# Performance work log

Hardware: AMD Instinct MI355X
Metric: run time of the kernel (lower is better)

Reference implementation:

```python
import jax, jax.numpy as jnp
import numpy as np

T, N, DEG = 8, 8192, 15
H = 4


def _gat(x, src, dst, wl, wr, a, b):
    """GATv2Conv with concat=False (heads averaged). x: [N, Cin] -> [N, Cout].
    e_ij = a_h . LeakyReLU(Wl x_j + Wr x_i); softmax over incoming edges of i;
    messages are Wl x_j (PyG GATv2 convention, self-loops already in edge list)."""
    n = x.shape[0]
    h, c = a.shape
    gl = (x @ wl).reshape(n, h, c)  # source-side transform
    gr = (x @ wr).reshape(n, h, c)  # target-side transform
    z = jax.nn.leaky_relu(gl[src] + gr[dst], 0.2)          # [E,H,C]
    e = jnp.einsum('ehc,hc->eh', z, a)                     # [E,H]
    m = jax.ops.segment_max(e, dst, num_segments=n)        # [N,H]
    ex = jnp.exp(e - m[dst])
    den = jax.ops.segment_sum(ex, dst, num_segments=n)     # [N,H]
    msg = jax.ops.segment_sum(ex[:, :, None] * gl[src], dst, num_segments=n)
    return (msg / den[:, :, None]).mean(axis=1) + b


def _d3(x, esrc, edst, wl, wr, a, b):
    # spatio-temporal graph conv: GATv2 applied independently per timestep
    return jax.lax.map(lambda args: _gat(args[0], args[1], args[2], wl, wr, a, b),
                       (x, esrc, edst))


def setup_inputs() -> dict:
    key = jax.random.key(0)
    ks = iter(jax.random.split(key, 32))
    x = jax.random.normal(next(ks), (T, N, 64), dtype=jnp.float32)
    # fixed-degree random graph per timestep + self loops (PyG add_self_loops=True)
    dst_base = jnp.repeat(jnp.arange(N, dtype=jnp.int32), DEG)
    src_r = jax.random.randint(next(ks), (T, N * DEG), 0, N, dtype=jnp.int32)
    loop = jnp.arange(N, dtype=jnp.int32)
    edge_src = jnp.concatenate([src_r, jnp.broadcast_to(loop, (T, N))], axis=1)
    edge_dst = jnp.concatenate([jnp.broadcast_to(dst_base, (T, N * DEG)),
                                jnp.broadcast_to(loop, (T, N))], axis=1)

    def gat_p(k, cin, cout):
        k1, k2, k3 = jax.random.split(k, 3)
        s = 1.0 / np.sqrt(cin)
        return ((jax.random.normal(k1, (cin, H * cout)) * s).astype(jnp.float32),
                (jax.random.normal(k2, (cin, H * cout)) * s).astype(jnp.float32),
                (jax.random.normal(k3, (H, cout)) * s).astype(jnp.float32),
                jnp.zeros((cout,), jnp.float32))

    inp = {"x": x, "edge_src": edge_src, "edge_dst": edge_dst}
    for name, cin, cout in [("c1", 64, 128), ("c2", 128, 64), ("c3", 64, 64), ("c4", 128, 64),
                            ("r11", 64, 64), ("r12", 64, 64), ("r2", 128, 128),
                            ("f11", 64, 64), ("f2", 128, 128)]:
        wl, wr, a, b = gat_p(next(ks), cin, cout)
        inp[name + "_wl"], inp[name + "_wr"], inp[name + "_a"], inp[name + "_b"] = wl, wr, a, b
    # ConvTranspose1d(k=1) == per-node linear conv_ch -> in_channels; then Linear in_channels -> original_dim
    for name, cin, cout in [("r3", 128, 64), ("f3", 128, 64), ("r4", 64, 64), ("f4", 64, 64)]:
        inp[name + "_w"] = (jax.random.normal(next(ks), (cin, cout)) * (1.0 / np.sqrt(cin))).astype(jnp.float32)
        inp[name + "_b"] = jnp.zeros((cout,), jnp.float32)
    return inp


def reference(x, edge_src, edge_dst,
              c1_wl, c1_wr, c1_a, c1_b, c2_wl, c2_wr, c2_a, c2_b,
              c3_wl, c3_wr, c3_a, c3_b, c4_wl, c4_wr, c4_a, c4_b,
              r11_wl, r11_wr, r11_a, r11_b, r12_wl, r12_wr, r12_a, r12_b,
              r2_wl, r2_wr, r2_a, r2_b, r3_w, r3_b, r4_w, r4_b,
              f11_wl, f11_wr, f11_a, f11_b, f2_wl, f2_wr, f2_a, f2_b,
              f3_w, f3_b, f4_w, f4_b):
    elu = jax.nn.elu
    out = elu(_d3(x, edge_src, edge_dst, c1_wl, c1_wr, c1_a, c1_b))           # [T,N,128]
    emb = elu(_d3(out, edge_src, edge_dst, c2_wl, c2_wr, c2_a, c2_b))         # [T,N,64]
    emb = elu(jnp.concatenate([_d3(emb, edge_src, edge_dst, c3_wl, c3_wr, c3_a, c3_b), emb], -1))  # [T,N,128]
    emb = elu(_d3(emb, edge_src, edge_dst, c4_wl, c4_wr, c4_a, c4_b))         # [T,N,64]

    # reconstruction branch on edges at t = -1
    s1, d1 = edge_src[-1], edge_dst[-1]
    r = elu(_gat(emb[-1], s1, d1, r11_wl, r11_wr, r11_a, r11_b))
    r = elu(jnp.concatenate([_gat(r, s1, d1, r12_wl, r12_wr, r12_a, r12_b), r], -1))  # [N,128]
    # F.dropout in eval mode -> identity
    r = elu(_gat(r, s1, d1, r2_wl, r2_wr, r2_a, r2_b))
    r = jnp.tanh(r @ r3_w + r3_b)
    recon = r @ r4_w + r4_b

    # forecasting branch on edges at t = -2 (original reuses reconstruct12 here)
    s2, d2 = edge_src[-2], edge_dst[-2]
    f = elu(_gat(emb[-2], s2, d2, f11_wl, f11_wr, f11_a, f11_b))
    f = elu(jnp.concatenate([_gat(f, s2, d2, r12_wl, r12_wr, r12_a, r12_b), f], -1))
    f = elu(_gat(f, s2, d2, f2_wl, f2_wr, f2_a, f2_b))
    f = jnp.tanh(f @ f3_w + f3_b)
    forecast = f @ f4_w + f4_b
    return (recon, forecast, emb)
```

## Files before the change

### kernel.cpp

```cpp
#include <hip/hip_runtime.h>
#include <cmath>

constexpr int T_   = 8;
constexpr int N_   = 8192;
constexpr int DEG_ = 15;
constexpr int E_   = N_ * (DEG_ + 1);
constexpr float L2E_ = 1.44269504f;

__device__ __forceinline__ float elu1(float v) {
  return v > 0.f ? v : exp2f(v * L2E_) - 1.f;
}

typedef __attribute__((ext_vector_type(8))) short bf16x8;
typedef __attribute__((ext_vector_type(4))) float f32x4;

__device__ __forceinline__ ushort f2bf(float x) {
  uint u = __float_as_uint(x);
  return (ushort)((u + 0x7FFFu + ((u >> 16) & 1u)) >> 16);
}
__device__ __forceinline__ float bf2f(ushort h) {
  return __uint_as_float(((uint)h) << 16);
}

template<int CTRL>
__device__ __forceinline__ float dpp_add(float x) {
  const int t = __builtin_amdgcn_mov_dpp(__float_as_int(x), CTRL, 0xf, 0xf, true);
  return x + __int_as_float(t);
}
__device__ __forceinline__ float row_reduce16(float x) {
  x = dpp_add<0x121>(x);
  x = dpp_add<0x122>(x);
  x = dpp_add<0x124>(x);
  x = dpp_add<0x128>(x);
  return x;
}

__global__ __launch_bounds__(256) void split_x(
    const float* __restrict__ X, ushort* __restrict__ XH, ushort* __restrict__ XL, int n4)
{
  const int i = blockIdx.x * 256 + threadIdx.x;
  if (i >= n4) return;
  const float4 v = ((const float4*)X)[i];
  const ushort h0 = f2bf(v.x), h1 = f2bf(v.y), h2 = f2bf(v.z), h3 = f2bf(v.w);
  ushort4 hh; hh.x = h0; hh.y = h1; hh.z = h2; hh.w = h3;
  ushort4 ll;
  ll.x = f2bf(v.x - bf2f(h0)); ll.y = f2bf(v.y - bf2f(h1));
  ll.z = f2bf(v.z - bf2f(h2)); ll.w = f2bf(v.w - bf2f(h3));
  ((ushort4*)XH)[i] = hh;
  ((ushort4*)XL)[i] = ll;
}

__global__ __launch_bounds__(256) void split_wt(
    const float* __restrict__ Wl, const float* __restrict__ Wr,
    ushort* __restrict__ WH, ushort* __restrict__ WL, int K, int HC)
{
  const int idx = blockIdx.x * 256 + threadIdx.x;
  if (idx >= 2 * HC * K) return;
  const int k = idx % K;
  const int n = (idx / K) % HC;
  const int s = idx / (K * HC);
  const float v = (s ? Wr : Wl)[k * HC + n];
  const ushort h = f2bf(v);
  WH[idx] = h;
  WL[idx] = f2bf(v - bf2f(h));
}

__global__ __launch_bounds__(256) void gemm_mfma(
    const ushort* __restrict__ Ah, const ushort* __restrict__ Al,
    const ushort* __restrict__ Wh, const ushort* __restrict__ Wl,
    float* __restrict__ Cl, float* __restrict__ Cr,
    int M, int Ncol, int K, int nt)
{
  __shared__ alignas(16) ushort lAh[4 * 1032];
  __shared__ alignas(16) ushort lAl[4 * 1032];
  __shared__ alignas(16) ushort lBh[4 * 520];
  __shared__ alignas(16) ushort lBl[4 * 520];

  const int z = blockIdx.z;
  const int t = (z < nt) ? z : z - nt;
  const int side = (z < nt) ? 0 : 1;
  const ushort* __restrict__ Bh = Wh + (size_t)side * Ncol * K;
  const ushort* __restrict__ Bl = Wl + (size_t)side * Ncol * K;
  float* __restrict__ C = (side ? Cr : Cl) + (size_t)t * M * Ncol;
  const size_t aoff = (size_t)t * M * K;

  const int bm = blockIdx.x * 128, bn = blockIdx.y * 64;
  const int tid = threadIdx.x;
  const int wid = tid >> 6, lane = tid & 63;
  const int l15 = lane & 15, lk = lane >> 4;

  f32x4 acc[2][4] = {};

  for (int k0 = 0; k0 < K; k0 += 32) {
    #pragma unroll
    for (int c = 0; c < 2; c++) {
      const int ch = tid + c * 256;
      const int row = ch >> 2, kc = ch & 3;
      const size_t ga = aoff + (size_t)(bm + row) * K + (k0 + kc * 8);
      *(uint4*)&lAh[kc * 1032 + row * 8] = *(const uint4*)(Ah + ga);
      *(uint4*)&lAl[kc * 1032 + row * 8] = *(const uint4*)(Al + ga);
    }
    {
      const int col = tid >> 2, kc = tid & 3;
      const size_t gb = (size_t)(bn + col) * K + (k0 + kc * 8);
      *(uint4*)&lBh[kc * 520 + col * 8] = *(const uint4*)(Bh + gb);
      *(uint4*)&lBl[kc * 520 + col * 8] = *(const uint4*)(Bl + gb);
    }
    __syncthreads();

    bf16x8 ah[2], al[2], bh4[4], bl4[4];
    const int r0 = wid * 32;
    #pragma unroll
    for (int rf = 0; rf < 2; rf++) {
      const int ro = (r0 + rf * 16 + l15) * 8;
      ah[rf] = *(const bf16x8*)&lAh[lk * 1032 + ro];
      al[rf] = *(const bf16x8*)&lAl[lk * 1032 + ro];
    }
    #pragma unroll
    for (int cf = 0; cf < 4; cf++) {
      const int co = (cf * 16 + l15) * 8;
      bh4[cf] = *(const bf16x8*)&lBh[lk * 520 + co];
      bl4[cf] = *(const bf16x8*)&lBl[lk * 520 + co];
    }
    #pragma unroll
    for (int rf = 0; rf < 2; rf++)
      #pragma unroll
      for (int cf = 0; cf < 4; cf++) {
        acc[rf][cf] = __builtin_amdgcn_mfma_f32_16x16x32_bf16(ah[rf], bh4[cf], acc[rf][cf], 0, 0, 0);
        acc[rf][cf] = __builtin_amdgcn_mfma_f32_16x16x32_bf16(ah[rf], bl4[cf], acc[rf][cf], 0, 0, 0);
        acc[rf][cf] = __builtin_amdgcn_mfma_f32_16x16x32_bf16(al[rf], bh4[cf], acc[rf][cf], 0, 0, 0);
      }
    __syncthreads();
  }

  #pragma unroll
  for (int rf = 0; rf < 2; rf++)
    #pragma unroll
    for (int cf = 0; cf < 4; cf++) {
      const int col = bn + cf * 16 + l15;
      #pragma unroll
      for (int reg = 0; reg < 4; reg++) {
        const int row = bm + wid * 32 + rf * 16 + lk * 4 + reg;
        C[(size_t)row * Ncol + col] = acc[rf][cf][reg];
      }
    }
}

template<int EPI>
__global__ __launch_bounds__(256) void gemm_k(
    const float* __restrict__ A, const float* __restrict__ B,
    float* __restrict__ C, const float* __restrict__ bias,
    int M, int Ncol, int K)
{
  __shared__ float As[16][68];
  __shared__ float Bs[16][64];

  const int tid = threadIdx.x;
  const int tx = tid & 15, ty = tid >> 4;
  const int bm = blockIdx.x * 64, bn = blockIdx.y * 64;

  const int arow = tid >> 2;
  const int akc  = (tid & 3) * 4;
  const int brow = tid >> 4;
  const int bc4  = (tid & 15) * 4;

  float acc[4][4];
  #pragma unroll
  for (int i = 0; i < 4; i++)
    #pragma unroll
    for (int j = 0; j < 4; j++) acc[i][j] = 0.f;

  for (int k0 = 0; k0 < K; k0 += 16) {
    const float4 va = *(const float4*)(A + (size_t)(bm + arow) * K + (k0 + akc));
    const float4 vb = *(const float4*)(B + (size_t)(k0 + brow) * Ncol + (bn + bc4));
    As[akc + 0][arow] = va.x; As[akc + 1][arow] = va.y;
    As[akc + 2][arow] = va.z; As[akc + 3][arow] = va.w;
    *(float4*)&Bs[brow][bc4] = vb;
    __syncthreads();
    #pragma unroll
    for (int kk = 0; kk < 16; kk++) {
      const float4 av = *(const float4*)&As[kk][ty * 4];
      const float4 bv = *(const float4*)&Bs[kk][tx * 4];
      const float a4[4] = {av.x, av.y, av.z, av.w};
      const float b4[4] = {bv.x, bv.y, bv.z, bv.w};
      #pragma unroll
      for (int i = 0; i < 4; i++)
        #pragma unroll
        for (int j = 0; j < 4; j++)
          acc[i][j] = fmaf(a4[i], b4[j], acc[i][j]);
    }
    __syncthreads();
  }

  #pragma unroll
  for (int i = 0; i < 4; i++) {
    const int row = bm + ty * 4 + i;
    const int col = bn + tx * 4;
    float v[4] = {acc[i][0], acc[i][1], acc[i][2], acc[i][3]};
    #pragma unroll
    for (int j = 0; j < 4; j++) v[j] += bias[col + j];
    if (EPI == 1) {
      #pragma unroll
      for (int j = 0; j < 4; j++) v[j] = tanhf(v[j]);
    }
    *(float4*)(C + (size_t)row * Ncol + col) = make_float4(v[0], v[1], v[2], v[3]);
  }
}

template<bool CONCAT, bool WF32>
__global__ __launch_bounds__(256) void gat_agg256(
    const float* __restrict__ GL, const float* __restrict__ GR,
    const float* __restrict__ aw_, const float* __restrict__ bias,
    const int* __restrict__ esrc, float* __restrict__ out,
    const float* __restrict__ csrc,
    ushort* __restrict__ SHo, ushort* __restrict__ SLo, int numNodes)
{
  constexpr int HC = 256, C = 64;
  constexpr int OSTR = CONCAT ? 128 : 64;

  const int lane = threadIdx.x & 63;
  const int wid  = threadIdx.x >> 6;
  const int t    = blockIdx.x >> 11;
  const int gid  = blockIdx.x * 4 + wid;
  if (gid >= numNodes) return;
  const int i = gid & (N_ - 1);

  const float* __restrict__ gl = GL + (size_t)t * N_ * HC;
  const int*   __restrict__ es = esrc + (size_t)t * E_ + (size_t)i * DEG_;
  const uint lo16 = (uint)lane << 4;

  float gr[4], a6[4], a4c[4];
  {
    const float4 gv = *(const float4*)(GR + (size_t)gid * HC + lane * 4);
    const float4 av = *(const float4*)(aw_ + lane * 4);
    gr[0] = gv.x; gr[1] = gv.y; gr[2] = gv.z; gr[3] = gv.w;
    a6[0] = 0.6f * L2E_ * av.x; a6[1] = 0.6f * L2E_ * av.y;
    a6[2] = 0.6f * L2E_ * av.z; a6[3] = 0.6f * L2E_ * av.w;
    a4c[0] = 0.4f * L2E_ * av.x; a4c[1] = 0.4f * L2E_ * av.y;
    a4c[2] = 0.4f * L2E_ * av.z; a4c[3] = 0.4f * L2E_ * av.w;
  }

  float acc[4] = {0.f, 0.f, 0.f, 0.f};
  float den = 0.f, m = -1e30f;

  #pragma unroll
  for (int b = 0; b < 4; b++) {
    uint off[4];
    #pragma unroll
    for (int q = 0; q < 4; q++) {
      const int ek = b * 4 + q;
      const uint j = (uint)((ek < DEG_) ? es[ek] : i);
      off[q] = (j << 10) + lo16;
    }
    float g[4][4];
    #pragma unroll
    for (int q = 0; q < 4; q++) {
      const float4 v = *(const float4*)((const char*)gl + off[q]);
      g[q][0] = v.x; g[q][1] = v.y; g[q][2] = v.z; g[q][3] = v.w;
    }
    float p[4];
    #pragma unroll
    for (int q = 0; q < 4; q++) {
      float s = 0.f;
      #pragma unroll
      for (int u = 0; u < 4; u++) {
        const float z = g[q][u] + gr[u];
        s = fmaf(z, a6[u], s);
        s = fmaf(fabsf(z), a4c[u], s);
      }
      p[q] = s;
    }
    #pragma unroll
    for (int q = 0; q < 4; q++) p[q] = row_reduce16(p[q]);

    const float bmax = fmaxf(fmaxf(p[0], p[1]), fmaxf(p[2], p[3]));
    const float nm   = fmaxf(m, bmax);
    const float sc   = exp2f(m - nm);
    den *= sc;
    #pragma unroll
    for (int u = 0; u < 4; u++) acc[u] *= sc;
    #pragma unroll
    for (int q = 0; q < 4; q++) {
      const float w = exp2f(p[q] - nm);
      den += w;
      #pragma unroll
      for (int u = 0; u < 4; u++) acc[u] = fmaf(w, g[q][u], acc[u]);
    }
    m = nm;
  }

  const float inv = 0.25f / den;
  #pragma unroll
  for (int u = 0; u < 4; u++) acc[u] *= inv;
  #pragma unroll
  for (int u = 0; u < 4; u++) {
    acc[u] += __shfl_xor(acc[u], 16);
    acc[u] += __shfl_xor(acc[u], 32);
  }

  if (lane < 16) {
    float o[4];
    #pragma unroll
    for (int u = 0; u < 4; u++)
      o[u] = elu1(acc[u] + bias[lane * 4 + u]);
    if (WF32)
      *(float4*)(out + (size_t)gid * OSTR + lane * 4) = make_float4(o[0], o[1], o[2], o[3]);
    ushort4 hh, ll;
    hh.x = f2bf(o[0]); hh.y = f2bf(o[1]); hh.z = f2bf(o[2]); hh.w = f2bf(o[3]);
    ll.x = f2bf(o[0] - bf2f(hh.x)); ll.y = f2bf(o[1] - bf2f(hh.y));
    ll.z = f2bf(o[2] - bf2f(hh.z)); ll.w = f2bf(o[3] - bf2f(hh.w));
    *(ushort4*)(SHo + (size_t)gid * OSTR + lane * 4) = hh;
    *(ushort4*)(SLo + (size_t)gid * OSTR + lane * 4) = ll;
  } else if (CONCAT && lane < 32) {
    const int q = lane - 16;
    const float4 v = *(const float4*)(csrc + (size_t)gid * C + q * 4);
    const float o0 = elu1(v.x), o1 = elu1(v.y), o2 = elu1(v.z), o3 = elu1(v.w);
    if (WF32)
      *(float4*)(out + (size_t)gid * OSTR + C + q * 4) = make_float4(o0, o1, o2, o3);
    ushort4 hh, ll;
    hh.x = f2bf(o0); hh.y = f2bf(o1); hh.z = f2bf(o2); hh.w = f2bf(o3);
    ll.x = f2bf(o0 - bf2f(hh.x)); ll.y = f2bf(o1 - bf2f(hh.y));
    ll.z = f2bf(o2 - bf2f(hh.z)); ll.w = f2bf(o3 - bf2f(hh.w));
    *(ushort4*)(SHo + (size_t)gid * OSTR + C + q * 4) = hh;
    *(ushort4*)(SLo + (size_t)gid * OSTR + C + q * 4) = ll;
  }
}

template<bool WF32, bool SPLIT>
__global__ __launch_bounds__(256) void gat_agg512(
    const float* __restrict__ GL, const float* __restrict__ GR,
    const float* __restrict__ aw_, const float* __restrict__ bias,
    const int* __restrict__ esrc, float* __restrict__ out,
    ushort* __restrict__ SHo, ushort* __restrict__ SLo)
{
  __shared__ float smem[4][128];

  const int lane = threadIdx.x & 63;
  const int h    = threadIdx.x >> 6;
  const int gid  = blockIdx.x;
  const int t = gid >> 13;
  const int i = gid & (N_ - 1);

  const float* __restrict__ gl = GL + (size_t)t * N_ * 512;
  const int*   __restrict__ es = esrc + (size_t)t * E_ + (size_t)i * DEG_;
  const int cb = h * 128 + lane * 2;
  const uint cbo = (uint)cb << 2;

  float gr0, gr1, a60, a61, a40, a41;
  {
    const float2 gv = *(const float2*)(GR + (size_t)gid * 512 + cb);
    const float2 av = *(const float2*)(aw_ + cb);
    gr0 = gv.x; gr1 = gv.y;
    a60 = 0.6f * L2E_ * av.x; a61 = 0.6f * L2E_ * av.y;
    a40 = 0.4f * L2E_ * av.x; a41 = 0.4f * L2E_ * av.y;
  }

  float acc0 = 0.f, acc1 = 0.f, den = 0.f, m = -1e30f;

  #pragma unroll
  for (int b = 0; b < 4; b++) {
    uint off[4];
    #pragma unroll
    for (int q = 0; q < 4; q++) {
      const int ek = b * 4 + q;
      const uint j = (uint)((ek < DEG_) ? es[ek] : i);
      off[q] = (j << 11) + cbo;
    }
    float g[4][2];
    #pragma unroll
    for (int q = 0; q < 4; q++) {
      const float2 v = *(const float2*)((const char*)gl + off[q]);
      g[q][0] = v.x; g[q][1] = v.y;
    }
    float p[4];
    #pragma unroll
    for (int q = 0; q < 4; q++) {
      const float z0 = g[q][0] + gr0;
      const float z1 = g[q][1] + gr1;
      float s = z0 * a60;
      s = fmaf(fabsf(z0), a40, s);
      s = fmaf(z1, a61, s);
      s = fmaf(fabsf(z1), a41, s);
      p[q] = s;
    }
    #pragma unroll
    for (int q = 0; q < 4; q++) {
      p[q] = row_reduce16(p[q]);
      p[q] += __shfl_xor(p[q], 16);
      p[q] += __shfl_xor(p[q], 32);
    }
    const float bmax = fmaxf(fmaxf(p[0], p[1]), fmaxf(p[2], p[3]));
    const float nm   = fmaxf(m, bmax);
    const float sc   = exp2f(m - nm);
    den *= sc; acc0 *= sc; acc1 *= sc;
    #pragma unroll
    for (int q = 0; q < 4; q++) {
      const float w = exp2f(p[q] - nm);
      den += w;
      acc0 = fmaf(w, g[q][0], acc0);
      acc1 = fmaf(w, g[q][1], acc1);
    }
    m = nm;
  }

  const float inv = 0.25f / den;
  smem[h][lane * 2]     = acc0 * inv;
  smem[h][lane * 2 + 1] = acc1 * inv;
  __syncthreads();

  if (h == 0) {
    const int c = lane * 2;
    float s0 = smem[0][c] + smem[1][c] + smem[2][c] + smem[3][c];
    float s1 = smem[0][c + 1] + smem[1][c + 1] + smem[2][c + 1] + smem[3][c + 1];
    s0 = elu1(s0 + bias[c]);
    s1 = elu1(s1 + bias[c + 1]);
    if (WF32)
      *(float2*)(out + (size_t)gid * 128 + c) = make_float2(s0, s1);
    if (SPLIT) {
      ushort2 hh, ll;
      hh.x = f2bf(s0); hh.y = f2bf(s1);
      ll.x = f2bf(s0 - bf2f(hh.x)); ll.y = f2bf(s1 - bf2f(hh.y));
      *(ushort2*)(SHo + (size_t)gid * 128 + c) = hh;
      *(ushort2*)(SLo + (size_t)gid * 128 + c) = ll;
    }
  }
}

extern "C" void kernel_launch(void* const* d_in, const int* in_sizes, int n_in,
                              void* d_out, int out_size, void* d_ws, size_t ws_size,
                              hipStream_t stream)
{
  (void)in_sizes; (void)n_in; (void)out_size; (void)ws_size;

  const float* x  = (const float*)d_in[0];
  const int*   es = (const int*)d_in[1];
  const float *c1_wl=(const float*)d_in[3], *c1_wr=(const float*)d_in[4], *c1_a=(const float*)d_in[5], *c1_b=(const float*)d_in[6];
  const float *c2_wl=(const float*)d_in[7], *c2_wr=(const float*)d_in[8], *c2_a=(const float*)d_in[9], *c2_b=(const float*)d_in[10];
  const float *c3_wl=(const float*)d_in[11],*c3_wr=(const float*)d_in[12],*c3_a=(const float*)d_in[13],*c3_b=(const float*)d_in[14];
  const float *c4_wl=(const float*)d_in[15],*c4_wr=(const float*)d_in[16],*c4_a=(const float*)d_in[17],*c4_b=(const float*)d_in[18];
  const float *r11_wl=(const float*)d_in[19],*r11_wr=(const float*)d_in[20],*r11_a=(const float*)d_in[21],*r11_b=(const float*)d_in[22];
  const float *r12_wl=(const float*)d_in[23],*r12_wr=(const float*)d_in[24],*r12_a=(const float*)d_in[25],*r12_b=(const float*)d_in[26];
  const float *r2_wl=(const float*)d_in[27],*r2_wr=(const float*)d_in[28],*r2_a=(const float*)d_in[29],*r2_b=(const float*)d_in[30];
  const float *f11_wl=(const float*)d_in[31],*f11_wr=(const float*)d_in[32],*f11_a=(const float*)d_in[33],*f11_b=(const float*)d_in[34];
  const float *f2_wl=(const float*)d_in[35],*f2_wr=(const float*)d_in[36],*f2_a=(const float*)d_in[37],*f2_b=(const float*)d_in[38];
  const float *r3_w=(const float*)d_in[39], *r3_b=(const float*)d_in[40];
  const float *f3_w=(const float*)d_in[41], *f3_b=(const float*)d_in[42];
  const float *r4_w=(const float*)d_in[43], *r4_b=(const float*)d_in[44];
  const float *f4_w=(const float*)d_in[45], *f4_b=(const float*)d_in[46];

  float* ws = (float*)d_ws;
  float* GL = ws;
  float* GR = GL + (size_t)16777216;
  float* A1 = GR + (size_t)16777216;
  float* B0 = A1 + (size_t)T_ * N_ * 64;
  float* B1 = B0 + (size_t)N_ * 128;
  ushort* SH  = (ushort*)(B1 + (size_t)N_ * 128);
  ushort* SL  = SH + (size_t)8388608;
  ushort* SH2 = SL + (size_t)8388608;
  ushort* SL2 = SH2 + (size_t)8388608;
  ushort* WH  = SL2 + (size_t)8388608;
  ushort* WL  = WH + (size_t)131072;

  float* recon = (float*)d_out;
  float* fcst  = recon + (size_t)N_ * 64;
  float* emb   = fcst + (size_t)N_ * 64;

  const dim3 blk(256);

  split_x<<<dim3(T_ * N_ * 64 / 4 / 256), blk, 0, stream>>>(x, SH, SL, T_ * N_ * 64 / 4);
  split_wt<<<dim3((2 * 512 * 64 + 255) / 256), blk, 0, stream>>>(c1_wl, c1_wr, WH, WL, 64, 512);
  for (int ch = 0; ch < 2; ch++) {
    const int t0 = ch * 4, nt = 4;
    gemm_mfma<<<dim3(N_ / 128, 8, 2 * nt), blk, 0, stream>>>(
        SH + (size_t)t0 * N_ * 64, SL + (size_t)t0 * N_ * 64, WH, WL, GL, GR, N_, 512, 64, nt);
    gat_agg512<false, true><<<dim3(nt * N_), blk, 0, stream>>>(
        GL, GR, c1_a, c1_b, es + (size_t)t0 * E_, nullptr,
        SH2 + (size_t)t0 * N_ * 128, SL2 + (size_t)t0 * N_ * 128);
  }
  split_wt<<<dim3((2 * 256 * 128 + 255) / 256), blk, 0, stream>>>(c2_wl, c2_wr, WH, WL, 128, 256);
  gemm_mfma<<<dim3(N_ / 128, 4, 2 * T_), blk, 0, stream>>>(SH2, SL2, WH, WL, GL, GR, N_, 256, 128, T_);
  gat_agg256<false, true><<<dim3(T_ * N_ / 4), blk, 0, stream>>>(
      GL, GR, c2_a, c2_b, es, A1, nullptr, SH, SL, T_ * N_);
  split_wt<<<dim3((2 * 256 * 64 + 255) / 256), blk, 0, stream>>>(c3_wl, c3_wr, WH, WL, 64, 256);
  gemm_mfma<<<dim3(N_ / 128, 4, 2 * T_), blk, 0, stream>>>(SH, SL, WH, WL, GL, GR, N_, 256, 64, T_);
  gat_agg256<true, false><<<dim3(T_ * N_ / 4), blk, 0, stream>>>(
      GL, GR, c3_a, c3_b, es, nullptr, A1, SH, SL, T_ * N_);
  split_wt<<<dim3((2 * 256 * 128 + 255) / 256), blk, 0, stream>>>(c4_wl, c4_wr, WH, WL, 128, 256);
  gemm_mfma<<<dim3(N_ / 128, 4, 2 * T_), blk, 0, stream>>>(SH, SL, WH, WL, GL, GR, N_, 256, 128, T_);
  gat_agg256<false, true><<<dim3(T_ * N_ / 4), blk, 0, stream>>>(
      GL, GR, c4_a, c4_b, es, emb, nullptr, SH2, SL2, T_ * N_);

  const int* esR = es + (size_t)7 * E_;
  split_wt<<<dim3((2 * 256 * 64 + 255) / 256), blk, 0, stream>>>(r11_wl, r11_wr, WH, WL, 64, 256);
  gemm_mfma<<<dim3(N_ / 128, 4, 2), blk, 0, stream>>>(
      SH2 + (size_t)7 * N_ * 64, SL2 + (size_t)7 * N_ * 64, WH, WL, GL, GR, N_, 256, 64, 1);
  gat_agg256<false, true><<<dim3(N_ / 4), blk, 0, stream>>>(
      GL, GR, r11_a, r11_b, esR, B0, nullptr, SH, SL, N_);
  split_wt<<<dim3((2 * 256 * 64 + 255) / 256), blk, 0, stream>>>(r12_wl, r12_wr, WH, WL, 64, 256);
  gemm_mfma<<<dim3(N_ / 128, 4, 2), blk, 0, stream>>>(SH, SL, WH, WL, GL, GR, N_, 256, 64, 1);
  gat_agg256<true, false><<<dim3(N_ / 4), blk, 0, stream>>>(
      GL, GR, r12_a, r12_b, esR, nullptr, B0, SH, SL, N_);
  split_wt<<<dim3((2 * 512 * 128 + 255) / 256), blk, 0, stream>>>(r2_wl, r2_wr, WH, WL, 128, 512);
  gemm_mfma<<<dim3(N_ / 128, 8, 2), blk, 0, stream>>>(SH, SL, WH, WL, GL, GR, N_, 512, 128, 1);
  gat_agg512<true, false><<<dim3(N_), blk, 0, stream>>>(GL, GR, r2_a, r2_b, esR, B0, nullptr, nullptr);
  gemm_k<1><<<dim3(N_ / 64, 1, 1), blk, 0, stream>>>(B0, r3_w, B1, r3_b, N_, 64, 128);
  gemm_k<2><<<dim3(N_ / 64, 1, 1), blk, 0, stream>>>(B1, r4_w, recon, r4_b, N_, 64, 64);

  const int* esF = es + (size_t)6 * E_;
  split_wt<<<dim3((2 * 256 * 64 + 255) / 256), blk, 0, stream>>>(f11_wl, f11_wr, WH, WL, 64, 256);
  gemm_mfma<<<dim3(N_ / 128, 4, 2), blk, 0, stream>>>(
      SH2 + (size_t)6 * N_ * 64, SL2 + (size_t)6 * N_ * 64, WH, WL, GL, GR, N_, 256, 64, 1);
  gat_agg256<false, true><<<dim3(N_ / 4), blk, 0, stream>>>(
      GL, GR, f11_a, f11_b, esF, B0, nullptr, SH, SL, N_);
  split_wt<<<dim3((2 * 256 * 64 + 255) / 256), blk, 0, stream>>>(r12_wl, r12_wr, WH, WL, 64, 256);
  gemm_mfma<<<dim3(N_ / 128, 4, 2), blk, 0, stream>>>(SH, SL, WH, WL, GL, GR, N_, 256, 64, 1);
  gat_agg256<true, false><<<dim3(N_ / 4), blk, 0, stream>>>(
      GL, GR, r12_a, r12_b, esF, nullptr, B0, SH, SL, N_);
  split_wt<<<dim3((2 * 512 * 128 + 255) / 256), blk, 0, stream>>>(f2_wl, f2_wr, WH, WL, 128, 512);
  gemm_mfma<<<dim3(N_ / 128, 8, 2), blk, 0, stream>>>(SH, SL, WH, WL, GL, GR, N_, 512, 128, 1);
  gat_agg512<true, false><<<dim3(N_), blk, 0, stream>>>(GL, GR, f2_a, f2_b, esF, B0, nullptr, nullptr);
  gemm_k<1><<<dim3(N_ / 64, 1, 1), blk, 0, stream>>>(B0, f3_w, B1, f3_b, N_, 64, 128);
  gemm_k<2><<<dim3(N_ / 64, 1, 1), blk, 0, stream>>>(B1, f4_w, fcst, f4_b, N_, 64, 64);
}
```

Baseline: 1.011 ms.

## Pad edge lists, batch weight splits, and remap 512-wide GAT aggregation to one wave per node

Adds a pre-pass that packs each node's 15 neighbours plus its self-loop into a 16-entry aligned array, so aggregation kernels load indices with uint4 reads instead of scalar loads and a branch. All nine weight bf16 hi/lo splits are merged into one launch with a table of offsets, which cuts many small kernel launches. gat_agg512 changes from a 4-wave block per node with a shared-memory head reduction to one wave per node, each lane covering 8 channels, which removes __syncthreads and LDS traffic. The online softmax skips the rescale on the first block. The cost is extra edge-index memory plus one more kernel, and higher register use in the 512 kernel.

```diff
diff --git a/kernel.cpp b/kernel.cpp
--- a/kernel.cpp
+++ b/kernel.cpp
@@ -33,6 +33,24 @@
   x = dpp_add<0x124>(x);
   x = dpp_add<0x128>(x);
   return x;
+}
+
+__global__ __launch_bounds__(256) void pad_edges(
+    const int* __restrict__ es, uint* __restrict__ es16, int total)
+{
+  const int idx = blockIdx.x * 256 + threadIdx.x;
+  if (idx >= total) return;
+  const int t = idx >> 13, i = idx & (N_ - 1);
+  const int* e = es + (size_t)t * E_ + (size_t)i * DEG_;
+  uint o[16];
+  #pragma unroll
+  for (int k = 0; k < DEG_; k++) o[k] = (uint)e[k];
+  o[15] = (uint)i;
+  uint4* dst = (uint4*)(es16 + (size_t)idx * 16);
+  dst[0] = make_uint4(o[0], o[1], o[2], o[3]);
+  dst[1] = make_uint4(o[4], o[5], o[6], o[7]);
+  dst[2] = make_uint4(o[8], o[9], o[10], o[11]);
+  dst[3] = make_uint4(o[12], o[13], o[14], o[15]);
 }
 
 __global__ __launch_bounds__(256) void split_x(
@@ -50,19 +68,26 @@
   ((ushort4*)XL)[i] = ll;
 }
 
-__global__ __launch_bounds__(256) void split_wt(
-    const float* __restrict__ Wl, const float* __restrict__ Wr,
-    ushort* __restrict__ WH, ushort* __restrict__ WL, int K, int HC)
-{
+struct WTable {
+  const float* wl[9]; const float* wr[9];
+  int lgK[9]; int lgHC[9]; int off[9];
+};
+__global__ __launch_bounds__(256) void split_wt_all(
+    WTable tb, ushort* __restrict__ WH, ushort* __restrict__ WL)
+{
+  const int y = blockIdx.y;
+  const int lgK = tb.lgK[y], lgHC = tb.lgHC[y];
+  const int n2 = 2 << (lgK + lgHC);
   const int idx = blockIdx.x * 256 + threadIdx.x;
-  if (idx >= 2 * HC * K) return;
-  const int k = idx % K;
-  const int n = (idx / K) % HC;
-  const int s = idx / (K * HC);
-  const float v = (s ? Wr : Wl)[k * HC + n];
+  if (idx >= n2) return;
+  const int k = idx & ((1 << lgK) - 1);
+  const int n = (idx >> lgK) & ((1 << lgHC) - 1);
+  const int s = idx >> (lgK + lgHC);
+  const float* W = s ? tb.wr[y] : tb.wl[y];
+  const float v = W[((size_t)k << lgHC) + n];
   const ushort h = f2bf(v);
-  WH[idx] = h;
-  WL[idx] = f2bf(v - bf2f(h));
+  WH[tb.off[y] + idx] = h;
+  WL[tb.off[y] + idx] = f2bf(v - bf2f(h));
 }
 
 __global__ __launch_bounds__(256) void gemm_mfma(
@@ -211,27 +236,25 @@
 __global__ __launch_bounds__(256) void gat_agg256(
     const float* __restrict__ GL, const float* __restrict__ GR,
     const float* __restrict__ aw_, const float* __restrict__ bias,
-    const int* __restrict__ esrc, float* __restrict__ out,
+    const uint* __restrict__ es16, float* __restrict__ out,
     const float* __restrict__ csrc,
-    ushort* __restrict__ SHo, ushort* __restrict__ SLo, int numNodes)
-{
-  constexpr int HC = 256, C = 64;
+    ushort* __restrict__ SHo, ushort* __restrict__ SLo)
+{
+  constexpr int C = 64;
   constexpr int OSTR = CONCAT ? 128 : 64;
 
   const int lane = threadIdx.x & 63;
   const int wid  = threadIdx.x >> 6;
   const int t    = blockIdx.x >> 11;
   const int gid  = blockIdx.x * 4 + wid;
-  if (gid >= numNodes) return;
-  const int i = gid & (N_ - 1);
-
-  const float* __restrict__ gl = GL + (size_t)t * N_ * HC;
-  const int*   __restrict__ es = esrc + (size_t)t * E_ + (size_t)i * DEG_;
+
+  const float* __restrict__ gl = GL + (size_t)t * N_ * 256;
+  const uint*  __restrict__ ep = es16 + (size_t)gid * 16;
   const uint lo16 = (uint)lane << 4;
 
   float gr[4], a6[4], a4c[4];
   {
-    const float4 gv = *(const float4*)(GR + (size_t)gid * HC + lane * 4);
+    const float4 gv = *(const float4*)(GR + (size_t)gid * 256 + lane * 4);
     const float4 av = *(const float4*)(aw_ + lane * 4);
     gr[0] = gv.x; gr[1] = gv.y; gr[2] = gv.z; gr[3] = gv.w;
     a6[0] = 0.6f * L2E_ * av.x; a6[1] = 0.6f * L2E_ * av.y;
@@ -241,17 +264,16 @@
   }
 
   float acc[4] = {0.f, 0.f, 0.f, 0.f};
-  float den = 0.f, m = -1e30f;
+  float den = 0.f, m = 0.f;
 
   #pragma unroll
   for (int b = 0; b < 4; b++) {
+    const uint4 j4 = *(const uint4*)(ep + b * 4);
     uint off[4];
-    #pragma unroll
-    for (int q = 0; q < 4; q++) {
-      const int ek = b * 4 + q;
-      const uint j = (uint)((ek < DEG_) ? es[ek] : i);
-      off[q] = (j << 10) + lo16;
-    }
+    off[0] = (j4.x << 10) + lo16;
+    off[1] = (j4.y << 10) + lo16;
+    off[2] = (j4.z << 10) + lo16;
+    off[3] = (j4.w << 10) + lo16;
     float g[4][4];
     #pragma unroll
     for (int q = 0; q < 4; q++) {
@@ -274,19 +296,23 @@
     for (int q = 0; q < 4; q++) p[q] = row_reduce16(p[q]);
 
     const float bmax = fmaxf(fmaxf(p[0], p[1]), fmaxf(p[2], p[3]));
-    const float nm   = fmaxf(m, bmax);
-    const float sc   = exp2f(m - nm);
-    den *= sc;
-    #pragma unroll
-    for (int u = 0; u < 4; u++) acc[u] *= sc;
+    if (b == 0) {
+      m = bmax;
+    } else {
+      const float nm = fmaxf(m, bmax);
+      const float sc = exp2f(m - nm);
+      den *= sc;
+      #pragma unroll
+      for (int u = 0; u < 4; u++) acc[u] *= sc;
+      m = nm;
+    }
     #pragma unroll
     for (int q = 0; q < 4; q++) {
-      const float w = exp2f(p[q] - nm);
+      const float w = exp2f(p[q] - m);
       den += w;
       #pragma unroll
       for (int u = 0; u < 4; u++) acc[u] = fmaf(w, g[q][u], acc[u]);
     }
-    m = nm;
   }
 
   const float inv = 0.25f / den;
@@ -330,98 +356,123 @@
 __global__ __launch_bounds__(256) void gat_agg512(
     const float* __restrict__ GL, const float* __restrict__ GR,
     const float* __restrict__ aw_, const float* __restrict__ bias,
-    const int* __restrict__ esrc, float* __restrict__ out,
+    const uint* __restrict__ es16, float* __restrict__ out,
     ushort* __restrict__ SHo, ushort* __restrict__ SLo)
 {
-  __shared__ float smem[4][128];
-
   const int lane = threadIdx.x & 63;
-  const int h    = threadIdx.x >> 6;
-  const int gid  = blockIdx.x;
-  const int t = gid >> 13;
-  const int i = gid & (N_ - 1);
+  const int wid  = threadIdx.x >> 6;
+  const int t    = blockIdx.x >> 11;
+  const int gid  = blockIdx.x * 4 + wid;
 
   const float* __restrict__ gl = GL + (size_t)t * N_ * 512;
-  const int*   __restrict__ es = esrc + (size_t)t * E_ + (size_t)i * DEG_;
-  const int cb = h * 128 + lane * 2;
-  const uint cbo = (uint)cb << 2;
-
-  float gr0, gr1, a60, a61, a40, a41;
+  const uint*  __restrict__ ep = es16 + (size_t)gid * 16;
+
+  const int s  = lane & 15;
+  const int cb = ((lane >> 4) << 7) + (s << 3);
+  const uint laneoff = (uint)cb << 2;
+
+  float gr[8], a6[8], a4[8];
   {
-    const float2 gv = *(const float2*)(GR + (size_t)gid * 512 + cb);
-    const float2 av = *(const float2*)(aw_ + cb);
-    gr0 = gv.x; gr1 = gv.y;
-    a60 = 0.6f * L2E_ * av.x; a61 = 0.6f * L2E_ * av.y;
-    a40 = 0.4f * L2E_ * av.x; a41 = 0.4f * L2E_ * av.y;
-  }
-
-  float acc0 = 0.f, acc1 = 0.f, den = 0.f, m = -1e30f;
+    const float4 g0 = *(const float4*)(GR + (size_t)gid * 512 + cb);
+    const float4 g1 = *(const float4*)(GR + (size_t)gid * 512 + cb + 4);
+    const float4 a0 = *(const float4*)(aw_ + cb);
+    const float4 a1 = *(const float4*)(aw_ + cb + 4);
+    gr[0] = g0.x; gr[1] = g0.y; gr[2] = g0.z; gr[3] = g0.w;
+    gr[4] = g1.x; gr[5] = g1.y; gr[6] = g1.z; gr[7] = g1.w;
+    a6[0] = 0.6f * L2E_ * a0.x; a6[1] = 0.6f * L2E_ * a0.y;
+    a6[2] = 0.6f * L2E_ * a0.z; a6[3] = 0.6f * L2E_ * a0.w;
+    a6[4] = 0.6f * L2E_ * a1.x; a6[5] = 0.6f * L2E_ * a1.y;
+    a6[6] = 0.6f * L2E_ * a1.z; a6[7] = 0.6f * L2E_ * a1.w;
+    a4[0] = 0.4f * L2E_ * a0.x; a4[1] = 0.4f * L2E_ * a0.y;
+    a4[2] = 0.4f * L2E_ * a0.z; a4[3] = 0.4f * L2E_ * a0.w;
+    a4[4] = 0.4f * L2E_ * a1.x; a4[5] = 0.4f * L2E_ * a1.y;
+    a4[6] = 0.4f * L2E_ * a1.z; a4[7] = 0.4f * L2E_ * a1.w;
+  }
+
+  float acc[8] = {0.f, 0.f, 0.f, 0.f, 0.f, 0.f, 0.f, 0.f};
+  float den = 0.f, m = 0.f;
 
   #pragma unroll
   for (int b = 0; b < 4; b++) {
+    const uint4 j4 = *(const uint4*)(ep + b * 4);
     uint off[4];
+    off[0] = (j4.x << 11) + laneoff;
+    off[1] = (j4.y << 11) + laneoff;
+    off[2] = (j4.z << 11) + laneoff;
+    off[3] = (j4.w << 11) + laneoff;
+    float g[4][8];
     #pragma unroll
     for (int q = 0; q < 4; q++) {
-      const int ek = b * 4 + q;
-      const uint j = (uint)((ek < DEG_) ? es[ek] : i);
-      off[q] = (j << 11) + cbo;
-    }
-    float g[4][2];
+      const float4 v0 = *(const float4*)((const char*)gl + off[q]);
+      const float4 v1 = *(const float4*)((const char*)gl + off[q] + 16);
+      g[q][0] = v0.x; g[q][1] = v0.y; g[q][2] = v0.z; g[q][3] = v0.w;
+      g[q][4] = v1.x; g[q][5] = v1.y; g[q][6] = v1.z; g[q][7] = v1.w;
+    }
+    float p[4];
     #pragma unroll
     for (int q = 0; q < 4; q++) {
-      const float2 v = *(const float2*)((const char*)gl + off[q]);
-      g[q][0] = v.x; g[q][1] = v.y;
-    }
-    float p[4];
+      float sc = 0.f;
+      #pragma unroll
+      for (int u = 0; u < 8; u++) {
+        const float z = g[q][u] + gr[u];
+        sc = fmaf(z, a6[u], sc);
+        sc = fmaf(fabsf(z), a4[u], sc);
+      }
+      p[q] = sc;
+    }
+    #pragma unroll
+    for (int q = 0; q < 4; q++) p[q] = row_reduce16(p[q]);
+
+    const float bmax = fmaxf(fmaxf(p[0], p[1]), fmaxf(p[2], p[3]));
+    if (b == 0) {
+      m = bmax;
+    } else {
+      const float nm = fmaxf(m, bmax);
+      const float sc = exp2f(m - nm);
+      den *= sc;
+      #pragma unroll
+      for (int u = 0; u < 8; u++) acc[u] *= sc;
+      m = nm;
+    }
     #pragma unroll
     for (int q = 0; q < 4; q++) {
-      const float z0 = g[q][0] + gr0;
-      const float z1 = g[q][1] + gr1;
-      float s = z0 * a60;
-      s = fmaf(fabsf(z0), a40, s);
-      s = fmaf(z1, a61, s);
-      s = fmaf(fabsf(z1), a41, s);
-      p[q] = s;
-    }
-    #pragma unroll
-    for (int q = 0; q < 4; q++) {
-      p[q] = row_reduce16(p[q]);
-      p[q] += __shfl_xor(p[q], 16);
-      p[q] += __shfl_xor(p[q], 32);
-    }
-    const float bmax = fmaxf(fmaxf(p[0], p[1]), fmaxf(p[2], p[3]));
-    const float nm   = fmaxf(m, bmax);
-    const float sc   = exp2f(m - nm);
-    den *= sc; acc0 *= sc; acc1 *= sc;
-    #pragma unroll
-    for (int q = 0; q < 4; q++) {
-      const float w = exp2f(p[q] - nm);
+      const float w = exp2f(p[q] - m);
       den += w;
-      acc0 = fmaf(w, g[q][0], acc0);
-      acc1 = fmaf(w, g[q][1], acc1);
-    }
-    m = nm;
+      #pragma unroll
+      for (int u = 0; u < 8; u++) acc[u] = fmaf(w, g[q][u], acc[u]);
+    }
   }
 
   const float inv = 0.25f / den;
-  smem[h][lane * 2]     = acc0 * inv;
-  smem[h][lane * 2 + 1] = acc1 * inv;
-  __syncthreads();
-
-  if (h == 0) {
-    const int c = lane * 2;
-    float s0 = smem[0][c] + smem[1][c] + smem[2][c] + smem[3][c];
-    float s1 = smem[0][c + 1] + smem[1][c + 1] + smem[2][c + 1] + smem[3][c + 1];
-    s0 = elu1(s0 + bias[c]);
-    s1 = elu1(s1 + bias[c + 1]);
-    if (WF32)
-      *(float2*)(out + (size_t)gid * 128 + c) = make_float2(s0, s1);
+  #pragma unroll
+  for (int u = 0; u < 8; u++) acc[u] *= inv;
+  #pragma unroll
+  for (int u = 0; u < 8; u++) {
+    acc[u] += __shfl_xor(acc[u], 16);
+    acc[u] += __shfl_xor(acc[u], 32);
+  }
+
+  if (lane < 16) {
+    float o[8];
+    #pragma unroll
+    for (int u = 0; u < 8; u++)
+      o[u] = elu1(acc[u] + bias[s * 8 + u]);
+    if (WF32) {
+      *(float4*)(out + (size_t)gid * 128 + s * 8)     = make_float4(o[0], o[1], o[2], o[3]);
+      *(float4*)(out + (size_t)gid * 128 + s * 8 + 4) = make_float4(o[4], o[5], o[6], o[7]);
+    }
     if (SPLIT) {
-      ushort2 hh, ll;
-      hh.x = f2bf(s0); hh.y = f2bf(s1);
-      ll.x = f2bf(s0 - bf2f(hh.x)); ll.y = f2bf(s1 - bf2f(hh.y));
-      *(ushort2*)(SHo + (size_t)gid * 128 + c) = hh;
-      *(ushort2*)(SLo + (size_t)gid * 128 + c) = ll;
+      ushort4 h0, h1, l0, l1;
+      h0.x = f2bf(o[0]); h0.y = f2bf(o[1]); h0.z = f2bf(o[2]); h0.w = f2bf(o[3]);
+      h1.x = f2bf(o[4]); h1.y = f2bf(o[5]); h1.z = f2bf(o[6]); h1.w = f2bf(o[7]);
+      l0.x = f2bf(o[0] - bf2f(h0.x)); l0.y = f2bf(o[1] - bf2f(h0.y));
+      l0.z = f2bf(o[2] - bf2f(h0.z)); l0.w = f2bf(o[3] - bf2f(h0.w));
+      l1.x = f2bf(o[4] - bf2f(h1.x)); l1.y = f2bf(o[5] - bf2f(h1.y));
+      l1.z = f2bf(o[6] - bf2f(h1.z)); l1.w = f2bf(o[7] - bf2f(h1.w));
+      *(ushort4*)(SHo + (size_t)gid * 128 + s * 8)     = h0;
+      *(ushort4*)(SHo + (size_t)gid * 128 + s * 8 + 4) = h1;
+      *(ushort4*)(SLo + (size_t)gid * 128 + s * 8)     = l0;
+      *(ushort4*)(SLo + (size_t)gid * 128 + s * 8 + 4) = l1;
     }
   }
 }
@@ -459,7 +510,8 @@
   ushort* SH2 = SL + (size_t)8388608;
   ushort* SL2 = SH2 + (size_t)8388608;
   ushort* WH  = SL2 + (size_t)8388608;
-  ushort* WL  = WH + (size_t)131072;
+  ushort* WL  = WH + (size_t)589824;
+  uint*  ES16 = (uint*)(WL + (size_t)589824);
 
   float* recon = (float*)d_out;
   float* fcst  = recon + (size_t)N_ * 64;
@@ -467,58 +519,75 @@
 
   const dim3 blk(256);
 
+  pad_edges<<<dim3(T_ * N_ / 256), blk, 0, stream>>>(es, ES16, T_ * N_);
   split_x<<<dim3(T_ * N_ * 64 / 4 / 256), blk, 0, stream>>>(x, SH, SL, T_ * N_ * 64 / 4);
-  split_wt<<<dim3((2 * 512 * 64 + 255) / 256), blk, 0, stream>>>(c1_wl, c1_wr, WH, WL, 64, 512);
+  WTable tb;
+  const float* wls[9] = {c1_wl, c2_wl, c3_wl, c4_wl, r11_wl, r12_wl, r2_wl, f11_wl, f2_wl};
+  const float* wrs[9] = {c1_wr, c2_wr, c3_wr, c4_wr, r11_wr, r12_wr, r2_wr, f11_wr, f2_wr};
+  const int Ks[9]  = {64, 128, 64, 128, 64, 64, 128, 64, 128};
+  const int HCs[9] = {512, 256, 256, 256, 256, 256, 512, 256, 512};
+  int woff[9]; int acc_off = 0;
+  for (int y = 0; y < 9; y++) {
+    tb.wl[y] = wls[y]; tb.wr[y] = wrs[y];
+    tb.lgK[y] = __builtin_ctz(Ks[y]); tb.lgHC[y] = __builtin_ctz(HCs[y]);
+    woff[y] = acc_off; tb.off[y] = acc_off;
+    acc_off += 2 * Ks[y] * HCs[y];
+  }
+  split_wt_all<<<dim3(512, 9), blk, 0, stream>>>(tb, WH, WL);
+
   for (int ch = 0; ch < 2; ch++) {
     const int t0 = ch * 4, nt = 4;
     gemm_mfma<<<dim3(N_ / 128, 8, 2 * nt), blk, 0, stream>>>(
-        SH + (size_t)t0 * N_ * 64, SL + (size_t)t0 * N_ * 64, WH, WL, GL, GR, N_, 512, 64, nt);
-    gat_agg512<false, true><<<dim3(nt * N_), blk, 0, stream>>>(
-        GL, GR, c1_a, c1_b, es + (size_t)t0 * E_, nullptr,
+        SH + (size_t)t0 * N_ * 64, SL + (size_t)t0 * N_ * 64,
+        WH + woff[0], WL + woff[0], GL, GR, N_, 512, 64, nt);
+    gat_agg512<false, true><<<dim3(nt * N_ / 4), blk, 0, stream>>>(
+        GL, GR, c1_a, c1_b, ES16 + (size_t)t0 * N_ * 16, nullptr,
         SH2 + (size_t)t0 * N_ * 128, SL2 + (size_t)t0 * N_ * 128);
   }
-  split_wt<<<dim3((2 * 256 * 128 + 255) / 256), blk, 0, stream>>>(c2_wl, c2_wr, WH, WL, 128, 256);
-  gemm_mfma<<<dim3(N_ / 128, 4, 2 * T_), blk, 0, stream>>>(SH2, SL2, WH, WL, GL, GR, N_, 256, 128, T_);
+  gemm_mfma<<<dim3(N_ / 128, 4, 2 * T_), blk, 0, stream>>>(
+      SH2, SL2, WH + woff[1], WL + woff[1], GL, GR, N_, 256, 128, T_);
   gat_agg256<false, true><<<dim3(T_ * N_ / 4), blk, 0, stream>>>(
-      GL, GR, c2_a, c2_b, es, A1, nullptr, SH, SL, T_ * N_);
-  split_wt<<<dim3((2 * 256 * 64 + 255) / 256), blk, 0, stream>>>(c3_wl, c3_wr, WH, WL, 64, 256);
-  gemm_mfma<<<dim3(N_ / 128, 4, 2 * T_), blk, 0, stream>>>(SH, SL, WH, WL, GL, GR, N_, 256, 64, T_);
+      GL, GR, c2_a, c2_b, ES16, A1, nullptr, SH, SL);
+  gemm_mfma<<<dim3(N_ / 128, 4, 2 * T_), blk, 0, stream>>>(
+      SH, SL, WH + woff[2], WL + woff[2], GL, GR, N_, 256, 64, T_);
   gat_agg256<true, false><<<dim3(T_ * N_ / 4), blk, 0, stream>>>(
-      GL, GR, c3_a, c3_b, es, nullptr, A1, SH, SL, T_ * N_);
-  split_wt<<<dim3((2 * 256 * 128 + 255) / 256), blk, 0, stream>>>(c4_wl, c4_wr, WH, WL, 128, 256);
-  gemm_mfma<<<dim3(N_ / 128, 4, 2 * T_), blk, 0, stream>>>(SH, SL, WH, WL, GL, GR, N_, 256, 128, T_);
+      GL, GR, c3_a, c3_b, ES16, nullptr, A1, SH, SL);
+  gemm_mfma<<<dim3(N_ / 128, 4, 2 * T_), blk, 0, stream>>>(
+      SH, SL, WH + woff[3], WL + woff[3], GL, GR, N_, 256, 128, T_);
   gat_agg256<false, true><<<dim3(T_ * N_ / 4), blk, 0, stream>>>(
-      GL, GR, c4_a, c4_b, es, emb, nullptr, SH2, SL2, T_ * N_);
-
-  const int* esR = es + (size_t)7 * E_;
-  split_wt<<<dim3((2 * 256 * 64 + 255) / 256), blk, 0, stream>>>(r11_wl, r11_wr, WH, WL, 64, 256);
+      GL, GR, c4_a, c4_b, ES16, emb, nullptr, SH2, SL2);
+
+  const uint* esR = ES16 + (size_t)7 * N_ * 16;
   gemm_mfma<<<dim3(N_ / 128, 4, 2), blk, 0, stream>>>(
-      SH2 + (size_t)7 * N_ * 64, SL2 + (size_t)7 * N_ * 64, WH, WL, GL, GR, N_, 256, 64, 1);
+      SH2 + (size_t)7 * N_ * 64, SL2 + (size_t)7 * N_ * 64,
+      WH + woff[4], WL + woff[4], GL, GR, N_, 256, 64, 1);
   gat_agg256<false, true><<<dim3(N_ / 4), blk, 0, stream>>>(
-      GL, GR, r11_a, r11_b, esR, B0, nullptr, SH, SL, N_);
-  split_wt<<<dim3((2 * 256 * 64 + 255) / 256), blk, 0, stream>>>(r12_wl, r12_wr, WH, WL, 64, 256);
-  gemm_mfma<<<dim3(N_ / 128, 4, 2), blk, 0, stream>>>(SH, SL, WH, WL, GL, GR, N_, 256, 64, 1);
+      GL, GR, r11_a, r11_b, esR, B0, nullptr, SH, SL);
+  gemm_mfma<<<dim3(N_ / 128, 4, 2), blk, 0, stream>>>(
+      SH, SL, WH + woff[5], WL + woff[5], GL, GR, N_, 256, 64, 1);
   gat_agg256<true, false><<<dim3(N_ / 4), blk, 0, stream>>>(
-      GL, GR, r12_a, r12_b, esR, nullptr, B0, SH, SL, N_);
-  split_wt<<<dim3((2 * 512 * 128 + 255) / 256), blk, 0, stream>>>(r2_wl, r2_wr, WH, WL, 128, 512);
-  gemm_mfma<<<dim3(N_ / 128, 8, 2), blk, 0, stream>>>(SH, SL, WH, WL, GL, GR, N_, 512, 128, 1);
-  gat_agg512<true, false><<<dim3(N_), blk, 0, stream>>>(GL, GR, r2_a, r2_b, esR, B0, nullptr, nullptr);
+      GL, GR, r12_a, r12_b, esR, nullptr, B0, SH, SL);
+  gemm_mfma<<<dim3(N_ / 128, 8, 2), blk, 0, stream>>>(
+      SH, SL, WH + woff[6], WL + woff[6], GL, GR, N_, 512, 128, 1);
+  gat_agg512<true, false><<<dim3(N_ / 4), blk, 0, stream>>>(
+      GL, GR, r2_a, r2_b, esR, B0, nullptr, nullptr);
   gemm_k<1><<<dim3(N_ / 64, 1, 1), blk, 0, stream>>>(B0, r3_w, B1, r3_b, N_, 64, 128);
   gemm_k<2><<<dim3(N_ / 64, 1, 1), blk, 0, stream>>>(B1, r4_w, recon, r4_b, N_, 64, 64);
 
-  const int* esF = es + (size_t)6 * E_;
-  split_wt<<<dim3((2 * 256 * 64 + 255) / 256), blk, 0, stream>>>(f11_wl, f11_wr, WH, WL, 64, 256);
+  const uint* esF = ES16 + (size_t)6 * N_ * 16;
   gemm_mfma<<<dim3(N_ / 128, 4, 2), blk, 0, stream>>>(
-      SH2 + (size_t)6 * N_ * 64, SL2 + (size_t)6 * N_ * 64, WH, WL, GL, GR, N_, 256, 64, 1);
+      SH2 + (size_t)6 * N_ * 64, SL2 + (size_t)6 * N_ * 64,
+      WH + woff[7], WL + woff[7], GL, GR, N_, 256, 64, 1);
   gat_agg256<false, true><<<dim3(N_ / 4), blk, 0, stream>>>(
-      GL, GR, f11_a, f11_b, esF, B0, nullptr, SH, SL, N_);
-  split_wt<<<dim3((2 * 256 * 64 + 255) / 256), blk, 0, stream>>>(r12_wl, r12_wr, WH, WL, 64, 256);
-  gemm_mfma<<<dim3(N_ / 128, 4, 2), blk, 0, stream>>>(SH, SL, WH, WL, GL, GR, N_, 256, 64, 1);
+      GL, GR, f11_a, f11_b, esF, B0, nullptr, SH, SL);
+  gemm_mfma<<<dim3(N_ / 128, 4, 2), blk, 0, stream>>>(
+      SH, SL, WH + woff[5], WL + woff[5], GL, GR, N_, 256, 64, 1);
   gat_agg256<true, false><<<dim3(N_ / 4), blk, 0, stream>>>(
-      GL, GR, r12_a, r12_b, esF, nullptr, B0, SH, SL, N_);
-  split_wt<<<dim3((2 * 512 * 128 + 255) / 256), blk, 0, stream>>>(f2_wl, f2_wr, WH, WL, 128, 512);
-  gemm_mfma<<<dim3(N_ / 128, 8, 2), blk, 0, stream>>>(SH, SL, WH, WL, GL, GR, N_, 512, 128, 1);
-  gat_agg512<true, false><<<dim3(N_), blk, 0, stream>>>(GL, GR, f2_a, f2_b, esF, B0, nullptr, nullptr);
+      GL, GR, r12_a, r12_b, esF, nullptr, B0, SH, SL);
+  gemm_mfma<<<dim3(N_ / 128, 8, 2), blk, 0, stream>>>(
+      SH, SL, WH + woff[8], WL + woff[8], GL, GR, N_, 512, 128, 1);
+  gat_agg512<true, false><<<dim3(N_ / 4), blk, 0, stream>>>(
+      GL, GR, f2_a, f2_b, esF, B0, nullptr, nullptr);
   gemm_k<1><<<dim3(N_ / 64, 1, 1), blk, 0, stream>>>(B0, f3_w, B1, f3_b, N_, 64, 128);
   gemm_k<2><<<dim3(N_ / 64, 1, 1), blk, 0, stream>>>(B1, f4_w, fcst, f4_b, N_, 64, 64);
 }
```

Result: no change. 1.001 ms (-1.0%).
